# Kernel optimization log

Hardware: AMD Instinct MI355X
Metric: run time of the kernel (lower is better)

Reference implementation:

```python
import jax, jax.numpy as jnp
import numpy as np

N, E, D, L, G = 100000, 300000, 256, 5, 4096


def _bn(x, p):
    # p: [4, dim] = (gamma, beta, running_mean, running_var); eval-mode BatchNorm1d
    g, b, m, v = p
    return (x - m) * jax.lax.rsqrt(v + 1e-5) * g + b


def setup_inputs() -> dict:
    key = jax.random.key(0)
    ks = iter(jax.random.split(key, 48))

    def nrm(shape, scale=0.02):
        return jax.random.normal(next(ks), shape, dtype=jnp.float32) * scale

    def bn_params(n, dim):
        g = 1.0 + nrm((n, dim), 0.1)
        b = nrm((n, dim), 0.1)
        m = nrm((n, dim), 0.1)
        v = 1.0 + jax.random.uniform(next(ks), (n, dim), dtype=jnp.float32)
        return jnp.stack([g, b, m, v], axis=1)  # [n,4,dim]

    return {
        "x": jax.random.randint(next(ks), (N, 9), 0, 2, dtype=jnp.int32),
        "edge_index": jax.random.randint(next(ks), (2, E), 0, N, dtype=jnp.int32),
        "edge_attr": jax.random.randint(next(ks), (E, 3), 0, 2, dtype=jnp.int32),
        "batch": jnp.sort(jax.random.randint(next(ks), (N,), 0, G, dtype=jnp.int32)),
        "atom_emb": nrm((9, 120, D)),            # AtomEncoder: 9 feature tables
        "bond_emb": nrm((L, 3, 6, D)),           # per-layer BondEncoder: 3 feature tables
        "vn0": jnp.zeros((D,), jnp.float32),     # virtualnode embedding (init 0)
        "eps": jnp.zeros((L,), jnp.float32),     # GIN eps per layer
        "conv_W1": nrm((L, D, 2 * D), 1.0 / np.sqrt(D)),     # GIN MLP (sampled BayesLinear)
        "conv_b1": nrm((L, 2 * D)),
        "conv_bn1": bn_params(L, 2 * D),
        "conv_W2": nrm((L, 2 * D, D), 1.0 / np.sqrt(2 * D)),
        "conv_b2": nrm((L, D)),
        "node_bn": bn_params(L, D),              # per-layer outer BatchNorm
        "vn_W1": nrm((L - 1, D, D), 1.0 / np.sqrt(D)),       # virtual-node MLP
        "vn_b1": nrm((L - 1, D)),
        "vn_bn1": bn_params(L - 1, D),
        "vn_W2": nrm((L - 1, D, D), 1.0 / np.sqrt(D)),
        "vn_b2": nrm((L - 1, D)),
        "vn_bn2": bn_params(L - 1, D),
    }


def reference(x, edge_index, edge_attr, batch, atom_emb, bond_emb, vn0, eps,
              conv_W1, conv_b1, conv_bn1, conv_W2, conv_b2, node_bn,
              vn_W1, vn_b1, vn_bn1, vn_W2, vn_b2, vn_bn2):
    src, dst = edge_index[0], edge_index[1]
    n_nodes = x.shape[0]
    n_layers = conv_W1.shape[0]
    # AtomEncoder: sum of 9 feature embeddings -> [N, D]
    h = atom_emb[jnp.arange(9), x].sum(axis=1)
    vn = jnp.broadcast_to(vn0, (G, vn0.shape[0]))  # [G, D]
    for l in range(n_layers):
        # broadcast virtual node into graph's nodes
        h = h + vn[batch]
        # GINConv: msg = relu(x_j + bond_emb), sum-aggregate, MLP((1+eps)x + aggr)
        e = bond_emb[l][jnp.arange(3), edge_attr].sum(axis=1)  # [E, D]
        msg = jax.nn.relu(h[src] + e)
        aggr = jax.ops.segment_sum(msg, dst, num_segments=n_nodes)
        t = (1.0 + eps[l]) * h + aggr
        t = jax.nn.relu(_bn(t @ conv_W1[l] + conv_b1[l], conv_bn1[l])) @ conv_W2[l] + conv_b2[l]
        hn = _bn(t, node_bn[l])  # outer BatchNorm (eval); dropout is identity in eval
        if l < n_layers - 1:
            hn = jax.nn.relu(hn)
            # global_add_pool of pre-conv h, then virtual-node MLP update
            vtemp = jax.ops.segment_sum(h, batch, num_segments=G) + vn
            u = jax.nn.relu(_bn(vtemp @ vn_W1[l] + vn_b1[l], vn_bn1[l]))
            vn = jax.nn.relu(_bn(u @ vn_W2[l] + vn_b2[l], vn_bn2[l]))
        h = hn
    return h  # JK == 'last'
```

## Files before the change

### kernel.cpp

```cpp
#include <hip/hip_runtime.h>

#define NN 100000
#define EE 300000
#define DD 256
#define LL 5
#define GG 4096
#define DB 512
#define MPAD 100096

typedef __attribute__((ext_vector_type(4))) float f32x4;
typedef __attribute__((ext_vector_type(8))) short s16x8;

__device__ __forceinline__ ushort f2bf(float f) {
  unsigned u = __float_as_uint(f);
  return (ushort)((u + 0x7fffu + ((u >> 16) & 1u)) >> 16);
}
__device__ __forceinline__ float b2f(ushort u) {
  return __uint_as_float(((unsigned)u) << 16);
}

__device__ __forceinline__ void gload16(const void* g, void* l) {
  __builtin_amdgcn_global_load_lds((const __attribute__((address_space(1))) void*)g,
                                   (__attribute__((address_space(3))) void*)l, 16, 0, 0);
}

__global__ void k_atom(const int* __restrict__ x, const float* __restrict__ emb,
                       const float* __restrict__ vn0, ushort* __restrict__ hvb) {
  int n = blockIdx.x * 4 + (threadIdx.x >> 6);
  if (n >= NN) return;
  int d = (threadIdx.x & 63) * 4;
  const float4 v0 = *(const float4*)&vn0[d];
  float ax = v0.x, ay = v0.y, az = v0.z, aw = v0.w;
#pragma unroll
  for (int f = 0; f < 9; ++f) {
    int v = x[n * 9 + f];
    const float4 t = *(const float4*)&emb[((size_t)(f * 120 + v)) * DD + d];
    ax += t.x; ay += t.y; az += t.z; aw += t.w;
  }
  ushort4 o; o.x = f2bf(ax); o.y = f2bf(ay); o.z = f2bf(az); o.w = f2bf(aw);
  *(ushort4*)&hvb[(size_t)n * DD + d] = o;
}

__global__ void k_vninit(const float* __restrict__ vn0, float* __restrict__ vn) {
  int i = blockIdx.x * blockDim.x + threadIdx.x;
  if (i < GG * DD) vn[i] = vn0[i & (DD - 1)];
}

__global__ void k_goff(const int* __restrict__ batch, int* __restrict__ goff) {
  int g = blockIdx.x * blockDim.x + threadIdx.x;
  if (g > GG) return;
  if (g == GG) { goff[GG] = NN; return; }
  int lo = 0, hi = NN;
  while (lo < hi) { int mid = (lo + hi) >> 1; if (batch[mid] < g) lo = mid + 1; else hi = mid; }
  goff[g] = lo;
}

__global__ void k_zero(int* __restrict__ p, int n) {
  int i = blockIdx.x * 256 + threadIdx.x;
  if (i < n) p[i] = 0;
}

__global__ void k_deg(const int* __restrict__ dst, int* __restrict__ deg) {
  int e = blockIdx.x * 256 + threadIdx.x;
  if (e < EE) atomicAdd(&deg[dst[e]], 1);
}

__global__ void k_scan1(const int* __restrict__ deg, int* __restrict__ coff,
                        int* __restrict__ bsum) {
  __shared__ int wsum[16];
  __shared__ int wpre[16];
  int lane = threadIdx.x & 63, wid = threadIdx.x >> 6;
  int i = blockIdx.x * 1024 + threadIdx.x;
  int v = (i < NN) ? deg[i] : 0;
  int xv = v;
#pragma unroll
  for (int off = 1; off < 64; off <<= 1) {
    int y = __shfl_up(xv, off);
    if (lane >= off) xv += y;
  }
  if (lane == 63) wsum[wid] = xv;
  __syncthreads();
  if (wid == 0 && lane < 16) {
    int s = wsum[lane];
    int xx = s;
#pragma unroll
    for (int off = 1; off < 16; off <<= 1) {
      int y = __shfl_up(xx, off);
      if (lane >= off) xx += y;
    }
    wpre[lane] = xx - s;
  }
  __syncthreads();
  int val = xv + wpre[wid];
  if (i < NN) coff[i + 1] = val;
  if (threadIdx.x == 1023) bsum[blockIdx.x] = val;
}

__global__ void k_scan2(int* __restrict__ bsum, int nb) {
  __shared__ int ws[2];
  int t = threadIdx.x, lane = t & 63, wid = t >> 6;
  int v = (t < nb) ? bsum[t] : 0;
  int xv = v;
#pragma unroll
  for (int off = 1; off < 64; off <<= 1) {
    int y = __shfl_up(xv, off);
    if (lane >= off) xv += y;
  }
  if (lane == 63) ws[wid] = xv;
  __syncthreads();
  int incl = xv + ((wid == 1) ? ws[0] : 0);
  if (t < nb) bsum[t] = incl - v;
}

__global__ void k_scan3(int* __restrict__ coff, const int* __restrict__ bpre) {
  int i = blockIdx.x * 1024 + threadIdx.x;
  if (i == 0) coff[0] = 0;
  if (i < NN) coff[i + 1] += bpre[i >> 10];
}

__global__ void k_eposinit(const int* __restrict__ coff, int* __restrict__ epos) {
  int n = blockIdx.x * 256 + threadIdx.x;
  if (n < NN) epos[n] = coff[n];
}

__global__ void k_scatter(const int* __restrict__ dst, int* __restrict__ epos,
                          int* __restrict__ eid) {
  int e = blockIdx.x * 256 + threadIdx.x;
  if (e < EE) { int p = atomicAdd(&epos[dst[e]], 1); eid[p] = e; }
}

__global__ void k_sort(const int* __restrict__ coff, int* __restrict__ eid) {
  int n = blockIdx.x * 256 + threadIdx.x;
  if (n >= NN) return;
  int s = coff[n], t = coff[n + 1];
  for (int i = s + 1; i < t; ++i) {
    int key = eid[i]; int j = i - 1;
    while (j >= s && eid[j] > key) { eid[j + 1] = eid[j]; --j; }
    eid[j + 1] = key;
  }
}

__global__ void k_emeta(const int* __restrict__ eid, const int* __restrict__ srcs,
                        const int* __restrict__ eattr, unsigned* __restrict__ emeta) {
  int idx = blockIdx.x * 256 + threadIdx.x;
  if (idx >= EE) return;
  int e = eid[idx];
  int s = srcs[e];
  unsigned c = (unsigned)(eattr[e * 3 + 0] + 2 * eattr[e * 3 + 1] + 4 * eattr[e * 3 + 2]);
  emeta[idx] = (unsigned)s | (c << 17);
}

__global__ void k_bond8(const float* __restrict__ bondE, float* __restrict__ bond8) {
  int l = blockIdx.x, c = blockIdx.y, d = threadIdx.x;
  float v = bondE[(((size_t)l * 3 + 0) * 6 + (c & 1)) * DD + d]
          + bondE[(((size_t)l * 3 + 1) * 6 + ((c >> 1) & 1)) * DD + d]
          + bondE[(((size_t)l * 3 + 2) * 6 + ((c >> 2) & 1)) * DD + d];
  bond8[((size_t)l * 8 + c) * DD + d] = v;
}

__global__ void k_wt(const float* __restrict__ in, ushort* __restrict__ out, int K, int N) {
  __shared__ float t[16][17];
  int l = blockIdx.z;
  int kb = blockIdx.x * 16, nb = blockIdx.y * 16;
  int tx = threadIdx.x & 15, ty = threadIdx.x >> 4;
  t[ty][tx] = in[(size_t)l * K * N + (size_t)(kb + ty) * N + nb + tx];
  __syncthreads();
  out[(size_t)l * N * K + (size_t)(nb + ty) * K + kb + tx] = f2bf(t[tx][ty]);
}

__global__ void k_pool(const ushort* __restrict__ hvb, const float* __restrict__ vn,
                       ushort* __restrict__ vtempb, const int* __restrict__ goff) {
  int g = blockIdx.x * 4 + (threadIdx.x >> 6);
  if (g >= GG) return;
  int d = (threadIdx.x & 63) * 4;
  float4 v = *(const float4*)&vn[(size_t)g * DD + d];
  float ax = v.x, ay = v.y, az = v.z, aw = v.w;
  int r0 = goff[g], r1 = goff[g + 1];
  for (int r = r0; r < r1; ++r) {
    ushort4 hu = *(const ushort4*)&hvb[(size_t)r * DD + d];
    ax += b2f(hu.x); ay += b2f(hu.y); az += b2f(hu.z); aw += b2f(hu.w);
  }
  ushort4 o; o.x = f2bf(ax); o.y = f2bf(ay); o.z = f2bf(az); o.w = f2bf(aw);
  *(ushort4*)&vtempb[(size_t)g * DD + d] = o;
}

__global__ void k_aggr(const ushort* __restrict__ hvb, ushort* __restrict__ tb,
                       const unsigned* __restrict__ emeta, const int* __restrict__ coff,
                       const float* __restrict__ bond8l, const float* __restrict__ epsp,
                       int l) {
  int n = blockIdx.x * 4 + (threadIdx.x >> 6);
  if (n >= NN) return;
  int d = (threadIdx.x & 63) * 4;
  float ax = 0.f, ay = 0.f, az = 0.f, aw = 0.f;
  int s0 = coff[n], s1 = coff[n + 1];
  int idx = s0;
  for (; idx + 2 <= s1; idx += 2) {
    unsigned m0 = emeta[idx], m1 = emeta[idx + 1];
    const ushort4 h0 = *(const ushort4*)&hvb[(size_t)(m0 & 0x1FFFFu) * DD + d];
    const ushort4 h1 = *(const ushort4*)&hvb[(size_t)(m1 & 0x1FFFFu) * DD + d];
    const float4 b0 = *(const float4*)&bond8l[(size_t)(m0 >> 17) * DD + d];
    const float4 b1 = *(const float4*)&bond8l[(size_t)(m1 >> 17) * DD + d];
    ax += fmaxf(b2f(h0.x) + b0.x, 0.f) + fmaxf(b2f(h1.x) + b1.x, 0.f);
    ay += fmaxf(b2f(h0.y) + b0.y, 0.f) + fmaxf(b2f(h1.y) + b1.y, 0.f);
    az += fmaxf(b2f(h0.z) + b0.z, 0.f) + fmaxf(b2f(h1.z) + b1.z, 0.f);
    aw += fmaxf(b2f(h0.w) + b0.w, 0.f) + fmaxf(b2f(h1.w) + b1.w, 0.f);
  }
  if (idx < s1) {
    unsigned m0 = emeta[idx];
    const ushort4 h0 = *(const ushort4*)&hvb[(size_t)(m0 & 0x1FFFFu) * DD + d];
    const float4 b0 = *(const float4*)&bond8l[(size_t)(m0 >> 17) * DD + d];
    ax += fmaxf(b2f(h0.x) + b0.x, 0.f);
    ay += fmaxf(b2f(h0.y) + b0.y, 0.f);
    az += fmaxf(b2f(h0.z) + b0.z, 0.f);
    aw += fmaxf(b2f(h0.w) + b0.w, 0.f);
  }
  float ep = 1.f + epsp[l];
  const ushort4 hn = *(const ushort4*)&hvb[(size_t)n * DD + d];
  ushort4 o;
  o.x = f2bf(ep * b2f(hn.x) + ax); o.y = f2bf(ep * b2f(hn.y) + ay);
  o.z = f2bf(ep * b2f(hn.z) + az); o.w = f2bf(ep * b2f(hn.w) + aw);
  *(ushort4*)&tb[(size_t)n * DD + d] = o;
}

template<int TM, int K, int NT>
__global__ __launch_bounds__(256) void k_gemm_f(
    const ushort* __restrict__ A, int M,
    const ushort* __restrict__ BT,
    void* __restrict__ Cv, int outBf16, int doRelu,
    const float* __restrict__ bias, const float* __restrict__ bn,
    const float* __restrict__ vnAdd, const int* __restrict__ batchv) {
  constexpr int KS = K / 8;
  constexpr int NK = K / 32;
  constexpr int NC = NT / 128;
  constexpr int MF = TM / 32;
  __shared__ ushort Alds[TM * K];
  __shared__ ushort Blds[2][128 * 32];
  const int tid = threadIdx.x;
  const int lane = tid & 63;
  const int w = tid >> 6;
  const int rowBase = blockIdx.x * TM;
  const int wrow = (w >> 1) * (TM / 2);
  const int wcol = (w & 1) * 64;
  const int r16 = lane & 15, kgrp = lane >> 4;

#pragma unroll
  for (int i = 0; i < TM * KS / 256; ++i) {
    int c = tid + i * 256;
    int row = c / KS, s = c % KS;
    int kg = s ^ (row & 7);
    gload16(A + (size_t)(rowBase + row) * K + kg * 8, (char*)Alds + c * 16);
  }
  const int bcol0 = tid >> 2, bkg0 = (tid & 3) ^ ((bcol0 >> 1) & 3);
  const int bcol1 = (tid + 256) >> 2, bkg1 = ((tid + 256) & 3) ^ ((bcol1 >> 1) & 3);
  auto stageB = [&](int pc, int pt, int b) {
    const ushort* base = BT + (size_t)pc * 128 * K + pt * 32;
    gload16(base + (size_t)bcol0 * K + bkg0 * 8, (char*)Blds[b] + tid * 16);
    gload16(base + (size_t)bcol1 * K + bkg1 * 8, (char*)Blds[b] + (tid + 256) * 16);
  };
  stageB(0, 0, 0);
  __syncthreads();

  int rbyte[MF], x7[MF];
#pragma unroll
  for (int m = 0; m < MF; ++m) {
    int row = wrow + m * 16 + r16;
    rbyte[m] = row * KS * 16;
    x7[m] = row & 7;
  }
  int boff[4];
#pragma unroll
  for (int n = 0; n < 4; ++n) {
    int col = wcol + n * 16 + r16;
    boff[n] = (col * 4 + (kgrp ^ ((col >> 1) & 3))) * 16;
  }

  f32x4 acc[MF][4];
#pragma unroll
  for (int m = 0; m < MF; ++m)
#pragma unroll
    for (int n = 0; n < 4; ++n) acc[m][n] = (f32x4)0.f;

  int cur = 0;
  for (int c = 0; c < NC; ++c) {
#pragma unroll
    for (int t = 0; t < NK; ++t) {
      if (t + 1 < NK) stageB(c, t + 1, cur ^ 1);
      else if (c + 1 < NC) stageB(c + 1, 0, cur ^ 1);
      s16x8 a[MF], b[4];
#pragma unroll
      for (int m = 0; m < MF; ++m)
        a[m] = *(const s16x8*)((const char*)Alds + rbyte[m] + ((((t << 2) + kgrp) ^ x7[m]) << 4));
#pragma unroll
      for (int n = 0; n < 4; ++n)
        b[n] = *(const s16x8*)((const char*)Blds[cur] + boff[n]);
#pragma unroll
      for (int m = 0; m < MF; ++m)
#pragma unroll
        for (int n = 0; n < 4; ++n)
          acc[m][n] = __builtin_amdgcn_mfma_f32_16x16x32_bf16(a[m], b[n], acc[m][n], 0, 0, 0);
      __syncthreads();
      cur ^= 1;
    }
    const int cb = c * 128;
    float alpha[4], beta[4];
#pragma unroll
    for (int n = 0; n < 4; ++n) {
      int col = cb + wcol + n * 16 + r16;
      float g = bn[col], bb = bn[NT + col], mm = bn[2 * NT + col], vv = bn[3 * NT + col];
      float s = g * rsqrtf(vv + 1e-5f);
      alpha[n] = s; beta[n] = fmaf(bias[col] - mm, s, bb);
    }
#pragma unroll
    for (int m = 0; m < MF; ++m) {
#pragma unroll
      for (int r = 0; r < 4; ++r) {
        int row = rowBase + wrow + m * 16 + kgrp * 4 + r;
        if (row < M) {
          const float* vp = vnAdd ? (vnAdd + (size_t)batchv[row] * NT) : nullptr;
#pragma unroll
          for (int n = 0; n < 4; ++n) {
            int col = cb + wcol + n * 16 + r16;
            float v = fmaf(acc[m][n][r], alpha[n], beta[n]);
            if (doRelu) v = fmaxf(v, 0.f);
            if (vp) v += vp[col];
            if (outBf16) ((ushort*)Cv)[(size_t)row * NT + col] = f2bf(v);
            else         ((float*)Cv)[(size_t)row * NT + col] = v;
          }
        }
      }
    }
#pragma unroll
    for (int m = 0; m < MF; ++m)
#pragma unroll
      for (int n = 0; n < 4; ++n) acc[m][n] = (f32x4)0.f;
  }
}

extern "C" void kernel_launch(void* const* d_in, const int* in_sizes, int n_in,
                              void* d_out, int out_size, void* d_ws, size_t ws_size,
                              hipStream_t stream) {
  const int*   x     = (const int*)d_in[0];
  const int*   ei    = (const int*)d_in[1];
  const int*   ea    = (const int*)d_in[2];
  const int*   batch = (const int*)d_in[3];
  const float* atomE = (const float*)d_in[4];
  const float* bondE = (const float*)d_in[5];
  const float* vn0   = (const float*)d_in[6];
  const float* eps   = (const float*)d_in[7];
  const float* cW1   = (const float*)d_in[8];
  const float* cb1   = (const float*)d_in[9];
  const float* cbn1  = (const float*)d_in[10];
  const float* cW2   = (const float*)d_in[11];
  const float* cb2   = (const float*)d_in[12];
  const float* nbn   = (const float*)d_in[13];
  const float* vW1   = (const float*)d_in[14];
  const float* vb1   = (const float*)d_in[15];
  const float* vbn1  = (const float*)d_in[16];
  const float* vW2   = (const float*)d_in[17];
  const float* vb2   = (const float*)d_in[18];
  const float* vbn2  = (const float*)d_in[19];
  (void)in_sizes; (void)n_in; (void)out_size; (void)ws_size;

  char* wsp = (char*)d_ws;
  size_t o = 0;
  auto alloc = [&](size_t bytes) -> char* {
    char* p = wsp + o; o += (bytes + 255) & ~(size_t)255; return p;
  };
  ushort* tbuf  = (ushort*)alloc((size_t)MPAD * DD * 2);
  ushort* c1b   = (ushort*)alloc((size_t)MPAD * DB * 2);
  float*  vn    = (float*) alloc((size_t)GG * DD * 4);
  ushort* vtmpb = (ushort*)alloc((size_t)GG * DD * 2);
  ushort* ub    = (ushort*)alloc((size_t)GG * DD * 2);
  ushort* bw1   = (ushort*)alloc((size_t)LL * DB * DD * 2);
  ushort* bw2   = (ushort*)alloc((size_t)LL * DD * DB * 2);
  ushort* bvw1  = (ushort*)alloc((size_t)(LL - 1) * DD * DD * 2);
  ushort* bvw2  = (ushort*)alloc((size_t)(LL - 1) * DD * DD * 2);
  float*  bond8 = (float*) alloc((size_t)LL * 8 * DD * 4);
  unsigned* emeta = (unsigned*)alloc((size_t)EE * 4);
  int* coff = (int*)alloc((size_t)(NN + 1) * 4);
  int* deg  = (int*)alloc((size_t)NN * 4);
  int* epos = (int*)alloc((size_t)NN * 4);
  int* eid  = (int*)alloc((size_t)EE * 4);
  int* goff = (int*)alloc((size_t)(GG + 1) * 4);
  int* bsum = (int*)alloc((size_t)128 * 4);

  const int* srcs = ei;
  const int* dsts = ei + EE;
  ushort* hvb = (ushort*)d_out;

  k_atom<<<(NN + 3) / 4, 256, 0, stream>>>(x, atomE, vn0, hvb);
  k_vninit<<<(GG * DD + 255) / 256, 256, 0, stream>>>(vn0, vn);
  k_goff<<<(GG + 256) / 256, 256, 0, stream>>>(batch, goff);
  k_zero<<<(NN + 255) / 256, 256, 0, stream>>>(deg, NN);
  k_deg<<<(EE + 255) / 256, 256, 0, stream>>>(dsts, deg);
  {
    int nb = (NN + 1023) / 1024;
    k_scan1<<<nb, 1024, 0, stream>>>(deg, coff, bsum);
    k_scan2<<<1, 128, 0, stream>>>(bsum, nb);
    k_scan3<<<nb, 1024, 0, stream>>>(coff, bsum);
  }
  k_eposinit<<<(NN + 255) / 256, 256, 0, stream>>>(coff, epos);
  k_scatter<<<(EE + 255) / 256, 256, 0, stream>>>(dsts, epos, eid);
  k_sort<<<(NN + 255) / 256, 256, 0, stream>>>(coff, eid);
  k_emeta<<<(EE + 255) / 256, 256, 0, stream>>>(eid, srcs, ea, emeta);
  k_bond8<<<dim3(LL, 8), 256, 0, stream>>>(bondE, bond8);
  k_wt<<<dim3(DD / 16, DB / 16, LL), 256, 0, stream>>>(cW1, bw1, DD, DB);
  k_wt<<<dim3(DB / 16, DD / 16, LL), 256, 0, stream>>>(cW2, bw2, DB, DD);
  k_wt<<<dim3(DD / 16, DD / 16, LL - 1), 256, 0, stream>>>(vW1, bvw1, DD, DD);
  k_wt<<<dim3(DD / 16, DD / 16, LL - 1), 256, 0, stream>>>(vW2, bvw2, DD, DD);

  for (int l = 0; l < LL; ++l) {
    if (l < LL - 1) {
      k_pool<<<(GG + 3) / 4, 256, 0, stream>>>(hvb, vn, vtmpb, goff);
      k_gemm_f<64, 256, 256><<<GG / 64, 256, 0, stream>>>(
          vtmpb, GG, bvw1 + (size_t)l * DD * DD, ub, 1, 1,
          vb1 + (size_t)l * DD, vbn1 + (size_t)l * 4 * DD, nullptr, nullptr);
      k_gemm_f<64, 256, 256><<<GG / 64, 256, 0, stream>>>(
          ub, GG, bvw2 + (size_t)l * DD * DD, vn, 0, 1,
          vb2 + (size_t)l * DD, vbn2 + (size_t)l * 4 * DD, nullptr, nullptr);
    }
    k_aggr<<<(NN + 3) / 4, 256, 0, stream>>>(hvb, tbuf, emeta, coff,
                                             bond8 + (size_t)l * 8 * DD, eps, l);
    k_gemm_f<128, 256, 512><<<MPAD / 128, 256, 0, stream>>>(
        tbuf, NN, bw1 + (size_t)l * DB * DD, c1b, 1, 1,
        cb1 + (size_t)l * DB, cbn1 + (size_t)l * 4 * DB, nullptr, nullptr);
    if (l < LL - 1) {
      k_gemm_f<64, 512, 256><<<MPAD / 64, 256, 0, stream>>>(
          c1b, NN, bw2 + (size_t)l * DD * DB, hvb, 1, 1,
          cb2 + (size_t)l * DD, nbn + (size_t)l * 4 * DD, vn, batch);
    } else {
      k_gemm_f<64, 512, 256><<<MPAD / 64, 256, 0, stream>>>(
          c1b, NN, bw2 + (size_t)l * DD * DB, (float*)d_out, 0, 0,
          cb2 + (size_t)l * DD, nbn + (size_t)l * 4 * DD, nullptr, nullptr);
    }
  }
}
```

Before: 1.398 ms.

## Fuse two-layer MLP GEMMs into one kernel keeping hidden activations in LDS

Replaces the pair of GEMM launches (W1 then W2) for both the GIN MLP and the virtual-node MLP with a single kernel. Each block computes a 64-row tile of the hidden layer, stores it as bf16 in swizzled LDS, then runs the second GEMM from LDS. This removes the global round trip of the N×512 intermediate and one launch per MLP. The first GEMM now reads A fragments straight from global memory instead of staging them in LDS, and tiles shrink to 64 rows, so there is less weight reuse per block and occupancy may drop because of the larger LDS footprint.

```diff
diff --git a/kernel.cpp b/kernel.cpp
--- a/kernel.cpp
+++ b/kernel.cpp
@@ -222,117 +222,161 @@
   *(ushort4*)&tb[(size_t)n * DD + d] = o;
 }
 
-template<int TM, int K, int NT>
-__global__ __launch_bounds__(256) void k_gemm_f(
+template<int K1, int N1, int N2>
+__global__ __launch_bounds__(256) void k_mlp(
     const ushort* __restrict__ A, int M,
-    const ushort* __restrict__ BT,
-    void* __restrict__ Cv, int outBf16, int doRelu,
-    const float* __restrict__ bias, const float* __restrict__ bn,
+    const ushort* __restrict__ W1T, const ushort* __restrict__ W2T,
+    const float* __restrict__ b1, const float* __restrict__ bn1,
+    const float* __restrict__ b2, const float* __restrict__ bn2,
+    void* __restrict__ Cv, int outBf16, int relu2,
     const float* __restrict__ vnAdd, const int* __restrict__ batchv) {
-  constexpr int KS = K / 8;
-  constexpr int NK = K / 32;
-  constexpr int NC = NT / 128;
-  constexpr int MF = TM / 32;
-  __shared__ ushort Alds[TM * K];
-  __shared__ ushort Blds[2][128 * 32];
+  constexpr int K2 = N1;
+  constexpr int TM = 64;
+  __shared__ ushort Wst[2][128 * 32];
+  __shared__ ushort c1s[TM * N1];
   const int tid = threadIdx.x;
   const int lane = tid & 63;
-  const int w = tid >> 6;
+  const int wv = tid >> 6;
+  const int wr = wv >> 1, wc = wv & 1;
+  const int r16 = lane & 15, kgrp = lane >> 4;
   const int rowBase = blockIdx.x * TM;
-  const int wrow = (w >> 1) * (TM / 2);
-  const int wcol = (w & 1) * 64;
-  const int r16 = lane & 15, kgrp = lane >> 4;
-
-#pragma unroll
-  for (int i = 0; i < TM * KS / 256; ++i) {
-    int c = tid + i * 256;
-    int row = c / KS, s = c % KS;
-    int kg = s ^ (row & 7);
-    gload16(A + (size_t)(rowBase + row) * K + kg * 8, (char*)Alds + c * 16);
-  }
-  const int bcol0 = tid >> 2, bkg0 = (tid & 3) ^ ((bcol0 >> 1) & 3);
-  const int bcol1 = (tid + 256) >> 2, bkg1 = ((tid + 256) & 3) ^ ((bcol1 >> 1) & 3);
-  auto stageB = [&](int pc, int pt, int b) {
-    const ushort* base = BT + (size_t)pc * 128 * K + pt * 32;
-    gload16(base + (size_t)bcol0 * K + bkg0 * 8, (char*)Blds[b] + tid * 16);
-    gload16(base + (size_t)bcol1 * K + bkg1 * 8, (char*)Blds[b] + (tid + 256) * 16);
-  };
-  stageB(0, 0, 0);
-  __syncthreads();
-
-  int rbyte[MF], x7[MF];
-#pragma unroll
-  for (int m = 0; m < MF; ++m) {
-    int row = wrow + m * 16 + r16;
-    rbyte[m] = row * KS * 16;
-    x7[m] = row & 7;
-  }
+
+  const int ca0 = tid, ca1 = tid + 256;
+  const int sc0 = ca0 >> 2, sk0 = (ca0 & 3) ^ ((sc0 >> 1) & 3);
+  const int sc1 = ca1 >> 2, sk1 = (ca1 & 3) ^ ((sc1 >> 1) & 3);
+
   int boff[4];
 #pragma unroll
   for (int n = 0; n < 4; ++n) {
-    int col = wcol + n * 16 + r16;
-    boff[n] = (col * 4 + (kgrp ^ ((col >> 1) & 3))) * 16;
-  }
-
-  f32x4 acc[MF][4];
-#pragma unroll
-  for (int m = 0; m < MF; ++m)
-#pragma unroll
-    for (int n = 0; n < 4; ++n) acc[m][n] = (f32x4)0.f;
-
-  int cur = 0;
-  for (int c = 0; c < NC; ++c) {
-#pragma unroll
-    for (int t = 0; t < NK; ++t) {
-      if (t + 1 < NK) stageB(c, t + 1, cur ^ 1);
-      else if (c + 1 < NC) stageB(c + 1, 0, cur ^ 1);
-      s16x8 a[MF], b[4];
-#pragma unroll
-      for (int m = 0; m < MF; ++m)
-        a[m] = *(const s16x8*)((const char*)Alds + rbyte[m] + ((((t << 2) + kgrp) ^ x7[m]) << 4));
-#pragma unroll
-      for (int n = 0; n < 4; ++n)
-        b[n] = *(const s16x8*)((const char*)Blds[cur] + boff[n]);
-#pragma unroll
-      for (int m = 0; m < MF; ++m)
+    int cl = wc * 64 + n * 16 + r16;
+    boff[n] = cl * 64 + ((kgrp ^ ((cl >> 1) & 3)) << 4);
+  }
+
+  const ushort* arow[2];
+#pragma unroll
+  for (int m = 0; m < 2; ++m)
+    arow[m] = A + (size_t)(rowBase + wr * 32 + m * 16 + r16) * K1 + kgrp * 8;
+
+  int arow2[2], ax7[2];
+#pragma unroll
+  for (int m = 0; m < 2; ++m) {
+    int rl = wr * 32 + m * 16 + r16;
+    arow2[m] = rl * (N1 * 2);
+    ax7[m] = rl & 7;
+  }
+
+  f32x4 acc[2][4];
+
+  for (int cc = 0; cc < N1 / 128; ++cc) {
+    const ushort* Wc = W1T + (size_t)cc * 128 * K1;
+    gload16(Wc + (size_t)sc0 * K1 + sk0 * 8, (char*)Wst[0] + ca0 * 16);
+    gload16(Wc + (size_t)sc1 * K1 + sk1 * 8, (char*)Wst[0] + ca1 * 16);
+#pragma unroll
+    for (int m = 0; m < 2; ++m)
+#pragma unroll
+      for (int n = 0; n < 4; ++n) acc[m][n] = (f32x4)0.f;
+    __syncthreads();
+    int cur = 0;
+    for (int t = 0; t < K1 / 32; ++t) {
+      if (t + 1 < K1 / 32) {
+        gload16(Wc + (size_t)sc0 * K1 + (t + 1) * 32 + sk0 * 8, (char*)Wst[cur ^ 1] + ca0 * 16);
+        gload16(Wc + (size_t)sc1 * K1 + (t + 1) * 32 + sk1 * 8, (char*)Wst[cur ^ 1] + ca1 * 16);
+      }
+      s16x8 a[2], b[4];
+#pragma unroll
+      for (int m = 0; m < 2; ++m) a[m] = *(const s16x8*)(arow[m] + t * 32);
+#pragma unroll
+      for (int n = 0; n < 4; ++n) b[n] = *(const s16x8*)((const char*)Wst[cur] + boff[n]);
+#pragma unroll
+      for (int m = 0; m < 2; ++m)
 #pragma unroll
         for (int n = 0; n < 4; ++n)
           acc[m][n] = __builtin_amdgcn_mfma_f32_16x16x32_bf16(a[m], b[n], acc[m][n], 0, 0, 0);
       __syncthreads();
       cur ^= 1;
     }
-    const int cb = c * 128;
-    float alpha[4], beta[4];
+    float al[4], be[4];
 #pragma unroll
     for (int n = 0; n < 4; ++n) {
-      int col = cb + wcol + n * 16 + r16;
-      float g = bn[col], bb = bn[NT + col], mm = bn[2 * NT + col], vv = bn[3 * NT + col];
+      int col = cc * 128 + wc * 64 + n * 16 + r16;
+      float g = bn1[col], bb = bn1[N1 + col], mm = bn1[2 * N1 + col], vv = bn1[3 * N1 + col];
       float s = g * rsqrtf(vv + 1e-5f);
-      alpha[n] = s; beta[n] = fmaf(bias[col] - mm, s, bb);
-    }
-#pragma unroll
-    for (int m = 0; m < MF; ++m) {
+      al[n] = s; be[n] = fmaf(b1[col] - mm, s, bb);
+    }
+#pragma unroll
+    for (int m = 0; m < 2; ++m) {
 #pragma unroll
       for (int r = 0; r < 4; ++r) {
-        int row = rowBase + wrow + m * 16 + kgrp * 4 + r;
+        int rl = wr * 32 + m * 16 + kgrp * 4 + r;
+        char* rowp = (char*)c1s + rl * (N1 * 2);
+        int x7 = rl & 7;
+#pragma unroll
+        for (int n = 0; n < 4; ++n) {
+          int col = cc * 128 + wc * 64 + n * 16 + r16;
+          float v = fmaxf(fmaf(acc[m][n][r], al[n], be[n]), 0.f);
+          int slot = (col >> 3) ^ x7;
+          *(ushort*)(rowp + slot * 16 + (col & 7) * 2) = f2bf(v);
+        }
+      }
+    }
+  }
+
+  for (int c2 = 0; c2 < N2 / 128; ++c2) {
+    const ushort* Wc = W2T + (size_t)c2 * 128 * K2;
+    gload16(Wc + (size_t)sc0 * K2 + sk0 * 8, (char*)Wst[0] + ca0 * 16);
+    gload16(Wc + (size_t)sc1 * K2 + sk1 * 8, (char*)Wst[0] + ca1 * 16);
+#pragma unroll
+    for (int m = 0; m < 2; ++m)
+#pragma unroll
+      for (int n = 0; n < 4; ++n) acc[m][n] = (f32x4)0.f;
+    __syncthreads();
+    int cur = 0;
+    for (int t = 0; t < K2 / 32; ++t) {
+      if (t + 1 < K2 / 32) {
+        gload16(Wc + (size_t)sc0 * K2 + (t + 1) * 32 + sk0 * 8, (char*)Wst[cur ^ 1] + ca0 * 16);
+        gload16(Wc + (size_t)sc1 * K2 + (t + 1) * 32 + sk1 * 8, (char*)Wst[cur ^ 1] + ca1 * 16);
+      }
+      s16x8 a[2], b[4];
+#pragma unroll
+      for (int m = 0; m < 2; ++m)
+        a[m] = *(const s16x8*)((const char*)c1s + arow2[m] + (((t * 4 + kgrp) ^ ax7[m]) << 4));
+#pragma unroll
+      for (int n = 0; n < 4; ++n) b[n] = *(const s16x8*)((const char*)Wst[cur] + boff[n]);
+#pragma unroll
+      for (int m = 0; m < 2; ++m)
+#pragma unroll
+        for (int n = 0; n < 4; ++n)
+          acc[m][n] = __builtin_amdgcn_mfma_f32_16x16x32_bf16(a[m], b[n], acc[m][n], 0, 0, 0);
+      __syncthreads();
+      cur ^= 1;
+    }
+    float al[4], be[4];
+#pragma unroll
+    for (int n = 0; n < 4; ++n) {
+      int col = c2 * 128 + wc * 64 + n * 16 + r16;
+      float g = bn2[col], bb = bn2[N2 + col], mm = bn2[2 * N2 + col], vv = bn2[3 * N2 + col];
+      float s = g * rsqrtf(vv + 1e-5f);
+      al[n] = s; be[n] = fmaf(b2[col] - mm, s, bb);
+    }
+#pragma unroll
+    for (int m = 0; m < 2; ++m) {
+#pragma unroll
+      for (int r = 0; r < 4; ++r) {
+        int row = rowBase + wr * 32 + m * 16 + kgrp * 4 + r;
         if (row < M) {
-          const float* vp = vnAdd ? (vnAdd + (size_t)batchv[row] * NT) : nullptr;
+          const float* vp = vnAdd ? (vnAdd + (size_t)batchv[row] * N2) : nullptr;
 #pragma unroll
           for (int n = 0; n < 4; ++n) {
-            int col = cb + wcol + n * 16 + r16;
-            float v = fmaf(acc[m][n][r], alpha[n], beta[n]);
-            if (doRelu) v = fmaxf(v, 0.f);
+            int col = c2 * 128 + wc * 64 + n * 16 + r16;
+            float v = fmaf(acc[m][n][r], al[n], be[n]);
+            if (relu2) v = fmaxf(v, 0.f);
             if (vp) v += vp[col];
-            if (outBf16) ((ushort*)Cv)[(size_t)row * NT + col] = f2bf(v);
-            else         ((float*)Cv)[(size_t)row * NT + col] = v;
+            if (outBf16) ((ushort*)Cv)[(size_t)row * N2 + col] = f2bf(v);
+            else         ((float*)Cv)[(size_t)row * N2 + col] = v;
           }
         }
       }
     }
-#pragma unroll
-    for (int m = 0; m < MF; ++m)
-#pragma unroll
-      for (int n = 0; n < 4; ++n) acc[m][n] = (f32x4)0.f;
   }
 }
 
@@ -367,10 +411,8 @@
     char* p = wsp + o; o += (bytes + 255) & ~(size_t)255; return p;
   };
   ushort* tbuf  = (ushort*)alloc((size_t)MPAD * DD * 2);
-  ushort* c1b   = (ushort*)alloc((size_t)MPAD * DB * 2);
   float*  vn    = (float*) alloc((size_t)GG * DD * 4);
   ushort* vtmpb = (ushort*)alloc((size_t)GG * DD * 2);
-  ushort* ub    = (ushort*)alloc((size_t)GG * DD * 2);
   ushort* bw1   = (ushort*)alloc((size_t)LL * DB * DD * 2);
   ushort* bw2   = (ushort*)alloc((size_t)LL * DD * DB * 2);
   ushort* bvw1  = (ushort*)alloc((size_t)(LL - 1) * DD * DD * 2);
@@ -412,26 +454,26 @@
   for (int l = 0; l < LL; ++l) {
     if (l < LL - 1) {
       k_pool<<<(GG + 3) / 4, 256, 0, stream>>>(hvb, vn, vtmpb, goff);
-      k_gemm_f<64, 256, 256><<<GG / 64, 256, 0, stream>>>(
-          vtmpb, GG, bvw1 + (size_t)l * DD * DD, ub, 1, 1,
-          vb1 + (size_t)l * DD, vbn1 + (size_t)l * 4 * DD, nullptr, nullptr);
-      k_gemm_f<64, 256, 256><<<GG / 64, 256, 0, stream>>>(
-          ub, GG, bvw2 + (size_t)l * DD * DD, vn, 0, 1,
-          vb2 + (size_t)l * DD, vbn2 + (size_t)l * 4 * DD, nullptr, nullptr);
+      k_mlp<256, 256, 256><<<GG / 64, 256, 0, stream>>>(
+          vtmpb, GG, bvw1 + (size_t)l * DD * DD, bvw2 + (size_t)l * DD * DD,
+          vb1 + (size_t)l * DD, vbn1 + (size_t)l * 4 * DD,
+          vb2 + (size_t)l * DD, vbn2 + (size_t)l * 4 * DD,
+          vn, 0, 1, nullptr, nullptr);
     }
     k_aggr<<<(NN + 3) / 4, 256, 0, stream>>>(hvb, tbuf, emeta, coff,
                                              bond8 + (size_t)l * 8 * DD, eps, l);
-    k_gemm_f<128, 256, 512><<<MPAD / 128, 256, 0, stream>>>(
-        tbuf, NN, bw1 + (size_t)l * DB * DD, c1b, 1, 1,
-        cb1 + (size_t)l * DB, cbn1 + (size_t)l * 4 * DB, nullptr, nullptr);
     if (l < LL - 1) {
-      k_gemm_f<64, 512, 256><<<MPAD / 64, 256, 0, stream>>>(
-          c1b, NN, bw2 + (size_t)l * DD * DB, hvb, 1, 1,
-          cb2 + (size_t)l * DD, nbn + (size_t)l * 4 * DD, vn, batch);
+      k_mlp<256, 512, 256><<<MPAD / 64, 256, 0, stream>>>(
+          tbuf, NN, bw1 + (size_t)l * DB * DD, bw2 + (size_t)l * DD * DB,
+          cb1 + (size_t)l * DB, cbn1 + (size_t)l * 4 * DB,
+          cb2 + (size_t)l * DD, nbn + (size_t)l * 4 * DD,
+          hvb, 1, 1, vn, batch);
     } else {
-      k_gemm_f<64, 512, 256><<<MPAD / 64, 256, 0, stream>>>(
-          c1b, NN, bw2 + (size_t)l * DD * DB, (float*)d_out, 0, 0,
-          cb2 + (size_t)l * DD, nbn + (size_t)l * 4 * DD, nullptr, nullptr);
-    }
-  }
-}
+      k_mlp<256, 512, 256><<<MPAD / 64, 256, 0, stream>>>(
+          tbuf, NN, bw1 + (size_t)l * DB * DD, bw2 + (size_t)l * DD * DB,
+          cb1 + (size_t)l * DB, cbn1 + (size_t)l * 4 * DB,
+          cb2 + (size_t)l * DD, nbn + (size_t)l * 4 * DD,
+          (float*)d_out, 0, 0, nullptr, nullptr);
+    }
+  }
+}
```

After: 1.257 ms. 10.1% less time.
